# Performance work log

Hardware: AMD Instinct MI355X
Metric: run time of the kernel (lower is better)

## Reference

```python
import jax, jax.numpy as jnp
import numpy as np

D_MODEL = 1024
D_HEAD = 64
B, S = 4, 2048


def setup_inputs() -> dict:
    key = jax.random.key(0)
    k1, k2, k3, k4 = jax.random.split(key, 4)
    residual_stream = jax.random.normal(k1, (B, S, D_MODEL), dtype=jnp.float32)
    # torch.nn.Linear weights are [out_features, in_features]
    Wq = jax.random.normal(k2, (D_HEAD, D_MODEL), dtype=jnp.float32) * 0.02
    Wk = jax.random.normal(k3, (D_HEAD, D_MODEL), dtype=jnp.float32) * 0.02
    Wv = jax.random.normal(k4, (D_HEAD, D_MODEL), dtype=jnp.float32) * 0.02
    return {"residual_stream": residual_stream, "Wq": Wq, "Wk": Wk, "Wv": Wv}


def reference(residual_stream, Wq, Wk, Wv):
    # Linear projections (no bias): y = x @ W.T
    q = jnp.einsum('bsd,hd->bsh', residual_stream, Wq)  # [B,S,d_head]
    k = jnp.einsum('bsd,hd->bsh', residual_stream, Wk)
    v = jnp.einsum('bsd,hd->bsh', residual_stream, Wv)
    # NOTE: module scales by 1/sqrt(d_model), not 1/sqrt(d_head)
    scale = 1.0 / jnp.sqrt(jnp.float32(D_MODEL))
    scores = jnp.einsum('bqh,bkh->bqk', q, k) * scale  # [B,S,S]
    # causal mask: lower-triangular allowed
    s = residual_stream.shape[1]
    causal = jnp.tril(jnp.ones((s, s), dtype=bool))
    scores = jnp.where(causal[None, :, :], scores, -jnp.inf)
    attn = jax.nn.softmax(scores, axis=-1)
    # dropout_chance=0.0 (eval/deterministic) -> identity
    return jnp.einsum('bqk,bkh->bqh', attn, v)  # [B,S,d_head]
```

## Files before the change

kernel.cpp:

```cpp
#include <hip/hip_runtime.h>
#include <hip/hip_bf16.h>

#define NB 4
#define SEQ 2048
#define DM 1024
#define DH 64

typedef __attribute__((ext_vector_type(8))) short bf16x8;
typedef __attribute__((ext_vector_type(4))) float f32x4;
typedef __attribute__((ext_vector_type(4))) short short4v;

__device__ inline short f2bf(float f) {
  union { float f; unsigned u; } x; x.f = f;
  unsigned r = x.u + 0x7FFFu + ((x.u >> 16) & 1u);
  return (short)(r >> 16);
}

__device__ inline float bf2f(short s) {
  union { unsigned u; float f; } x;
  x.u = ((unsigned)(unsigned short)s) << 16;
  return x.f;
}

__global__ __launch_bounds__(256) void wconv_kernel(
    const float* __restrict__ Wq, const float* __restrict__ Wk,
    const float* __restrict__ Wv, short* __restrict__ wbf)
{
  const int tid = blockIdx.x * 256 + threadIdx.x;
  const int base = tid * 8;
  const int row = base >> 10;
  const int col = base & 1023;
  const float* src = (row < 64) ? Wq : (row < 128) ? Wk : Wv;
  src += (size_t)(row & 63) * DM + col;
  f32x4 f0 = ((const f32x4*)src)[0];
  f32x4 f1 = ((const f32x4*)src)[1];
  bf16x8 h = { f2bf(f0[0]), f2bf(f0[1]), f2bf(f0[2]), f2bf(f0[3]),
               f2bf(f1[0]), f2bf(f1[1]), f2bf(f1[2]), f2bf(f1[3]) };
  *(bf16x8*)(wbf + (size_t)row * DM + col) = h;
}

__global__ __launch_bounds__(512) void proj_v3_kernel(
    const float* __restrict__ X, const short* __restrict__ wbf,
    short* __restrict__ pacc)
{
  __shared__ short w_lds[192][264];
  __shared__ short x_lds[2][32][264];

  const int t = threadIdx.x;
  const int l = t & 63;
  const int w = t >> 6;
  const int ks = blockIdx.y;
  const int kbase = ks * 256;
  const int mbase = blockIdx.x * 128;

#pragma unroll
  for (int i = 0; i < 12; i++) {
    const int idx = t + i * 512;
    const int row = idx >> 5;
    const int cb = idx & 31;
    *(bf16x8*)&w_lds[row][cb * 8] =
        *(const bf16x8*)(wbf + (size_t)row * DM + kbase + cb * 8);
  }

  const int xr0 = t >> 6;
  const int xc0 = (t & 63) * 4;

  f32x4 xp0, xp1, xp2, xp3;
  {
    const float* base = X + (size_t)(mbase + xr0) * DM + kbase + xc0;
    xp0 = *(const f32x4*)(base + 0 * 8 * DM);
    xp1 = *(const f32x4*)(base + 1 * 8 * DM);
    xp2 = *(const f32x4*)(base + 2 * 8 * DM);
    xp3 = *(const f32x4*)(base + 3 * 8 * DM);
  }
  {
    short4v h0 = { f2bf(xp0[0]), f2bf(xp0[1]), f2bf(xp0[2]), f2bf(xp0[3]) };
    short4v h1 = { f2bf(xp1[0]), f2bf(xp1[1]), f2bf(xp1[2]), f2bf(xp1[3]) };
    short4v h2 = { f2bf(xp2[0]), f2bf(xp2[1]), f2bf(xp2[2]), f2bf(xp2[3]) };
    short4v h3 = { f2bf(xp3[0]), f2bf(xp3[1]), f2bf(xp3[2]), f2bf(xp3[3]) };
    *(short4v*)&x_lds[0][xr0 + 0][xc0]  = h0;
    *(short4v*)&x_lds[0][xr0 + 8][xc0]  = h1;
    *(short4v*)&x_lds[0][xr0 + 16][xc0] = h2;
    *(short4v*)&x_lds[0][xr0 + 24][xc0] = h3;
  }
  __syncthreads();

  const int arow = (w & 1) * 16 + (l & 15);
  const int kk = (l >> 4) << 3;
  const int cg = (w >> 1) * 3;
  short* pp = pacc + (size_t)ks * (NB * SEQ) * 192;

#pragma unroll
  for (int mt = 0; mt < 4; mt++) {
    const int buf = mt & 1;

    if (mt < 3) {
      const float* base = X + (size_t)(mbase + (mt + 1) * 32 + xr0) * DM + kbase + xc0;
      xp0 = *(const f32x4*)(base + 0 * 8 * DM);
      xp1 = *(const f32x4*)(base + 1 * 8 * DM);
      xp2 = *(const f32x4*)(base + 2 * 8 * DM);
      xp3 = *(const f32x4*)(base + 3 * 8 * DM);
    }

    f32x4 acc0 = (f32x4){0.f, 0.f, 0.f, 0.f};
    f32x4 acc1 = (f32x4){0.f, 0.f, 0.f, 0.f};
    f32x4 acc2 = (f32x4){0.f, 0.f, 0.f, 0.f};
#pragma unroll
    for (int k8 = 0; k8 < 8; k8++) {
      const int kc = k8 * 32 + kk;
      bf16x8 a  = *(const bf16x8*)&x_lds[buf][arow][kc];
      bf16x8 b0 = *(const bf16x8*)&w_lds[(cg + 0) * 16 + (l & 15)][kc];
      acc0 = __builtin_amdgcn_mfma_f32_16x16x32_bf16(a, b0, acc0, 0, 0, 0);
      bf16x8 b1 = *(const bf16x8*)&w_lds[(cg + 1) * 16 + (l & 15)][kc];
      acc1 = __builtin_amdgcn_mfma_f32_16x16x32_bf16(a, b1, acc1, 0, 0, 0);
      bf16x8 b2 = *(const bf16x8*)&w_lds[(cg + 2) * 16 + (l & 15)][kc];
      acc2 = __builtin_amdgcn_mfma_f32_16x16x32_bf16(a, b2, acc2, 0, 0, 0);
    }

    {
      const int rowb = mbase + mt * 32 + (w & 1) * 16 + ((l >> 4) << 2);
      const int c0 = (cg + 0) * 16 + (l & 15);
      const int c1 = (cg + 1) * 16 + (l & 15);
      const int c2 = (cg + 2) * 16 + (l & 15);
#pragma unroll
      for (int j = 0; j < 4; j++) {
        pp[(size_t)(rowb + j) * 192 + c0] = f2bf(acc0[j]);
        pp[(size_t)(rowb + j) * 192 + c1] = f2bf(acc1[j]);
        pp[(size_t)(rowb + j) * 192 + c2] = f2bf(acc2[j]);
      }
    }

    if (mt < 3) {
      short4v h0 = { f2bf(xp0[0]), f2bf(xp0[1]), f2bf(xp0[2]), f2bf(xp0[3]) };
      short4v h1 = { f2bf(xp1[0]), f2bf(xp1[1]), f2bf(xp1[2]), f2bf(xp1[3]) };
      short4v h2 = { f2bf(xp2[0]), f2bf(xp2[1]), f2bf(xp2[2]), f2bf(xp2[3]) };
      short4v h3 = { f2bf(xp3[0]), f2bf(xp3[1]), f2bf(xp3[2]), f2bf(xp3[3]) };
      *(short4v*)&x_lds[buf ^ 1][xr0 + 0][xc0]  = h0;
      *(short4v*)&x_lds[buf ^ 1][xr0 + 8][xc0]  = h1;
      *(short4v*)&x_lds[buf ^ 1][xr0 + 16][xc0] = h2;
      *(short4v*)&x_lds[buf ^ 1][xr0 + 24][xc0] = h3;
    }
    __syncthreads();
  }
}

__global__ __launch_bounds__(256) void reduce4_kernel(
    const short* __restrict__ pacc, short* __restrict__ qout,
    short* __restrict__ kout, short* __restrict__ vtout)
{
  const int gid = blockIdx.x * 256 + threadIdx.x;
  const int r = gid / 48;
  const int cg = gid - r * 48;
  const int c0 = cg * 4;

  float v0 = 0.f, v1 = 0.f, v2 = 0.f, v3 = 0.f;
#pragma unroll
  for (int s = 0; s < 4; s++) {
    const short4v a = *(const short4v*)(pacc + ((size_t)s * (NB * SEQ) + r) * 192 + c0);
    v0 += bf2f(a[0]); v1 += bf2f(a[1]); v2 += bf2f(a[2]); v3 += bf2f(a[3]);
  }

  if (c0 < 64) {
    short4v h = { f2bf(v0 * 0.03125f), f2bf(v1 * 0.03125f),
                  f2bf(v2 * 0.03125f), f2bf(v3 * 0.03125f) };
    *(short4v*)(qout + (size_t)r * DH + c0) = h;
  } else if (c0 < 128) {
    short4v h = { f2bf(v0), f2bf(v1), f2bf(v2), f2bf(v3) };
    *(short4v*)(kout + (size_t)r * DH + (c0 - 64)) = h;
  } else {
    const int bb = r >> 11, s = r & (SEQ - 1);
    short* vt = vtout + (size_t)bb * DH * SEQ + (size_t)(c0 - 128) * SEQ + s;
    vt[0 * SEQ] = f2bf(v0);
    vt[1 * SEQ] = f2bf(v1);
    vt[2 * SEQ] = f2bf(v2);
    vt[3 * SEQ] = f2bf(v3);
  }
}

__global__ __launch_bounds__(512) void proj_fb_kernel(
    const float* __restrict__ X, const short* __restrict__ wbf,
    short* __restrict__ qout, short* __restrict__ kout,
    short* __restrict__ vtout)
{
  __shared__ short x_lds[2][32][80];
  __shared__ short w_lds[2][192][80];

  const int t = threadIdx.x;
  const int l = t & 63;
  const int w = t >> 6;
  const int m0 = blockIdx.x * 32;

  f32x4 acc[3];
#pragma unroll
  for (int i = 0; i < 3; i++) acc[i] = (f32x4){0.f, 0.f, 0.f, 0.f};

  const int xr = t >> 4;
  const int xc = (t & 15) * 4;
  const int wr = t >> 3;
  const int wc = (t & 7) * 8;

  const float* xsrc  = X   + (size_t)(m0 + xr) * DM + xc;
  const short* wsrc0 = wbf + (size_t)(wr)       * DM + wc;
  const short* wsrc1 = wbf + (size_t)(64 + wr)  * DM + wc;
  const short* wsrc2 = wbf + (size_t)(128 + wr) * DM + wc;

  {
    f32x4 f = *(const f32x4*)xsrc;
    short4v h = { f2bf(f[0]), f2bf(f[1]), f2bf(f[2]), f2bf(f[3]) };
    *(short4v*)&x_lds[0][xr][xc] = h;
    *(bf16x8*)&w_lds[0][wr][wc]       = *(const bf16x8*)wsrc0;
    *(bf16x8*)&w_lds[0][64 + wr][wc]  = *(const bf16x8*)wsrc1;
    *(bf16x8*)&w_lds[0][128 + wr][wc] = *(const bf16x8*)wsrc2;
  }
  f32x4 xA = *(const f32x4*)(xsrc + 64);
  bf16x8 wA0 = *(const bf16x8*)(wsrc0 + 64);
  bf16x8 wA1 = *(const bf16x8*)(wsrc1 + 64);
  bf16x8 wA2 = *(const bf16x8*)(wsrc2 + 64);
  f32x4 xB;
  bf16x8 wB0, wB1, wB2;
  __syncthreads();

#pragma unroll
  for (int it = 0; it < 16; it++) {
    const int buf = it & 1;
    const int k2 = (it + 2) * 64;

    if ((it & 1) == 0) {
      if (it + 2 < 16) {
        xB  = *(const f32x4*)(xsrc + k2);
        wB0 = *(const bf16x8*)(wsrc0 + k2);
        wB1 = *(const bf16x8*)(wsrc1 + k2);
        wB2 = *(const bf16x8*)(wsrc2 + k2);
      }
    } else {
      if (it + 2 < 16) {
        xA  = *(const f32x4*)(xsrc + k2);
        wA0 = *(const bf16x8*)(wsrc0 + k2);
        wA1 = *(const bf16x8*)(wsrc1 + k2);
        wA2 = *(const bf16x8*)(wsrc2 + k2);
      }
    }

    const short* xp = &x_lds[buf][(w & 1) * 16 + (l & 15)][(l >> 4) << 3];
    bf16x8 a0 = *(const bf16x8*)xp;
    bf16x8 a1 = *(const bf16x8*)(xp + 32);
#pragma unroll
    for (int nf = 0; nf < 3; nf++) {
      const int cf = (w >> 1) * 3 + nf;
      const short* wp = &w_lds[buf][cf * 16 + (l & 15)][(l >> 4) << 3];
      bf16x8 b0 = *(const bf16x8*)wp;
      bf16x8 b1 = *(const bf16x8*)(wp + 32);
      acc[nf] = __builtin_amdgcn_mfma_f32_16x16x32_bf16(a0, b0, acc[nf], 0, 0, 0);
      acc[nf] = __builtin_amdgcn_mfma_f32_16x16x32_bf16(a1, b1, acc[nf], 0, 0, 0);
    }

    if (it < 15) {
      if ((it & 1) == 0) {
        short4v h = { f2bf(xA[0]), f2bf(xA[1]), f2bf(xA[2]), f2bf(xA[3]) };
        *(short4v*)&x_lds[buf ^ 1][xr][xc] = h;
        *(bf16x8*)&w_lds[buf ^ 1][wr][wc]       = wA0;
        *(bf16x8*)&w_lds[buf ^ 1][64 + wr][wc]  = wA1;
        *(bf16x8*)&w_lds[buf ^ 1][128 + wr][wc] = wA2;
      } else {
        short4v h = { f2bf(xB[0]), f2bf(xB[1]), f2bf(xB[2]), f2bf(xB[3]) };
        *(short4v*)&x_lds[buf ^ 1][xr][xc] = h;
        *(bf16x8*)&w_lds[buf ^ 1][wr][wc]       = wB0;
        *(bf16x8*)&w_lds[buf ^ 1][64 + wr][wc]  = wB1;
        *(bf16x8*)&w_lds[buf ^ 1][128 + wr][wc] = wB2;
      }
    }
    __syncthreads();
  }

  const int rowb = m0 + (w & 1) * 16 + ((l >> 4) << 2);
#pragma unroll
  for (int nf = 0; nf < 3; nf++) {
    const int c = ((w >> 1) * 3 + nf) * 16 + (l & 15);
#pragma unroll
    for (int j = 0; j < 4; j++) {
      const int row = rowb + j;
      const float v = acc[nf][j];
      if (c < 64) {
        qout[row * DH + c] = f2bf(v * 0.03125f);
      } else if (c < 128) {
        kout[row * DH + (c - 64)] = f2bf(v);
      } else {
        const int b = row >> 11, s = row & (SEQ - 1);
        vtout[b * (DH * SEQ) + (c - 128) * SEQ + s] = f2bf(v);
      }
    }
  }
}

__global__ __launch_bounds__(256) void flash_kernel(
    const short* __restrict__ qin, const short* __restrict__ kin,
    const short* __restrict__ vtin, float* __restrict__ po,
    float* __restrict__ pm, float* __restrict__ pl,
    const int nck, const int cht)
{
  __shared__ short k_lds[2][64][72];
  __shared__ short vt_lds[2][64][72];
  __shared__ short p_lds[4][16][72];

  const int qt = blockIdx.x;
  const int ck = blockIdx.y;
  const int t0 = ck * cht;
  if (t0 > qt) return;
  const int b = blockIdx.z;

  const int t = threadIdx.x;
  const int l = t & 63;
  const int w = t >> 6;
  const int q0 = qt * 64;
  const int tend = min(t0 + cht, qt + 1);

  const short* qb = qin  + (size_t)b * SEQ * DH;
  const short* kb = kin  + (size_t)b * SEQ * DH;
  const short* vb = vtin + (size_t)b * DH * SEQ;

  const short* qr = qb + (size_t)(q0 + w * 16 + (l & 15)) * DH + ((l >> 4) << 3);
  const bf16x8 qf0 = *(const bf16x8*)qr;
  const bf16x8 qf1 = *(const bf16x8*)(qr + 32);

  f32x4 o[4];
#pragma unroll
  for (int i = 0; i < 4; i++) o[i] = (f32x4){0.f, 0.f, 0.f, 0.f};
  float m_run[4] = {-1e30f, -1e30f, -1e30f, -1e30f};
  float l_run[4] = {0.f, 0.f, 0.f, 0.f};

  const int sr = t >> 3;
  const int sc = (t & 7) * 8;

  {
    const int j0 = t0 * 64;
#pragma unroll
    for (int i = 0; i < 2; i++) {
      const int r = sr + i * 32;
      *(bf16x8*)&k_lds[0][r][sc]  = *(const bf16x8*)(kb + (size_t)(j0 + r) * DH + sc);
      *(bf16x8*)&vt_lds[0][r][sc] = *(const bf16x8*)(vb + (size_t)r * SEQ + j0 + sc);
    }
  }
  __syncthreads();

  for (int tt = t0; tt < tend; tt++) {
    const int bi = (tt - t0) & 1;
    const int j0 = tt * 64;
    const bool pf = (tt + 1 < tend);

    bf16x8 kpf0, kpf1, vpf0, vpf1;
    if (pf) {
      const int j1 = j0 + 64;
      kpf0 = *(const bf16x8*)(kb + (size_t)(j1 + sr) * DH + sc);
      kpf1 = *(const bf16x8*)(kb + (size_t)(j1 + sr + 32) * DH + sc);
      vpf0 = *(const bf16x8*)(vb + (size_t)sr * SEQ + j1 + sc);
      vpf1 = *(const bf16x8*)(vb + (size_t)(sr + 32) * SEQ + j1 + sc);
    }

    f32x4 s[4];
#pragma unroll
    for (int nf = 0; nf < 4; nf++) {
      const short* kr = &k_lds[bi][nf * 16 + (l & 15)][(l >> 4) << 3];
      bf16x8 b0 = *(const bf16x8*)kr;
      bf16x8 b1 = *(const bf16x8*)(kr + 32);
      f32x4 a = (f32x4){0.f, 0.f, 0.f, 0.f};
      a = __builtin_amdgcn_mfma_f32_16x16x32_bf16(qf0, b0, a, 0, 0, 0);
      a = __builtin_amdgcn_mfma_f32_16x16x32_bf16(qf1, b1, a, 0, 0, 0);
      s[nf] = a;
    }

    {
      const int growb = q0 + w * 16 + ((l >> 4) << 2);
#pragma unroll
      for (int nf = 0; nf < 4; nf++) {
        const int gcol = j0 + nf * 16 + (l & 15);
#pragma unroll
        for (int j = 0; j < 4; j++)
          if (gcol > growb + j) s[nf][j] = -1e30f;
      }
    }

    float alpha[4];
#pragma unroll
    for (int j = 0; j < 4; j++) {
      float tm = fmaxf(fmaxf(s[0][j], s[1][j]), fmaxf(s[2][j], s[3][j]));
      tm = fmaxf(tm, __shfl_xor(tm, 1));
      tm = fmaxf(tm, __shfl_xor(tm, 2));
      tm = fmaxf(tm, __shfl_xor(tm, 4));
      tm = fmaxf(tm, __shfl_xor(tm, 8));
      const float mn = fmaxf(m_run[j], tm);
      alpha[j] = exp2f((m_run[j] - mn) * 1.44269504f);
      m_run[j] = mn;
      float rs = 0.f;
#pragma unroll
      for (int nf = 0; nf < 4; nf++) {
        const float p = exp2f((s[nf][j] - mn) * 1.44269504f);
        s[nf][j] = p;
        rs += p;
      }
      rs += __shfl_xor(rs, 1);
      rs += __shfl_xor(rs, 2);
      rs += __shfl_xor(rs, 4);
      rs += __shfl_xor(rs, 8);
      l_run[j] = l_run[j] * alpha[j] + rs;
    }
#pragma unroll
    for (int df = 0; df < 4; df++)
#pragma unroll
      for (int j = 0; j < 4; j++) o[df][j] *= alpha[j];

#pragma unroll
    for (int nf = 0; nf < 4; nf++)
#pragma unroll
      for (int j = 0; j < 4; j++)
        p_lds[w][((l >> 4) << 2) + j][nf * 16 + (l & 15)] = f2bf(s[nf][j]);

    asm volatile("s_waitcnt lgkmcnt(0)" ::: "memory");
    __builtin_amdgcn_sched_barrier(0);

#pragma unroll
    for (int ks = 0; ks < 2; ks++) {
      const short* pr = &p_lds[w][l & 15][ks * 32 + ((l >> 4) << 3)];
      const bf16x8 pa = *(const bf16x8*)pr;
#pragma unroll
      for (int df = 0; df < 4; df++) {
        const short* vr = &vt_lds[bi][df * 16 + (l & 15)][ks * 32 + ((l >> 4) << 3)];
        const bf16x8 vf = *(const bf16x8*)vr;
        o[df] = __builtin_amdgcn_mfma_f32_16x16x32_bf16(pa, vf, o[df], 0, 0, 0);
      }
    }

    if (pf) {
      *(bf16x8*)&k_lds[bi ^ 1][sr][sc]       = kpf0;
      *(bf16x8*)&k_lds[bi ^ 1][sr + 32][sc]  = kpf1;
      *(bf16x8*)&vt_lds[bi ^ 1][sr][sc]      = vpf0;
      *(bf16x8*)&vt_lds[bi ^ 1][sr + 32][sc] = vpf1;
    }
    __syncthreads();
  }

  const int rowb = q0 + w * 16 + ((l >> 4) << 2);
#pragma unroll
  for (int j = 0; j < 4; j++) {
    const size_t rowg = (size_t)b * SEQ + rowb + j;
#pragma unroll
    for (int df = 0; df < 4; df++)
      po[(rowg * nck + ck) * DH + df * 16 + (l & 15)] = o[df][j];
    if ((l & 15) == 0) {
      pm[rowg * nck + ck] = m_run[j];
      pl[rowg * nck + ck] = l_run[j];
    }
  }
}

__global__ __launch_bounds__(256) void merge_kernel(
    const float* __restrict__ po, const float* __restrict__ pm,
    const float* __restrict__ pl, float* __restrict__ out,
    const int nck, const int ckshift)
{
  const int gid = blockIdx.x * 256 + threadIdx.x;
  const int r = gid >> 6;
  const int d = gid & 63;
  const int s = r & (SEQ - 1);
  const int C = (s >> ckshift) + 1;

  float m = -1e30f;
  for (int c = 0; c < C; c++) m = fmaxf(m, pm[r * nck + c]);
  float den = 0.f, num = 0.f;
  for (int c = 0; c < C; c++) {
    const float wgt = exp2f((pm[r * nck + c] - m) * 1.44269504f);
    den += pl[r * nck + c] * wgt;
    num += po[(size_t)(r * nck + c) * DH + d] * wgt;
  }
  out[gid] = num / den;
}

extern "C" void kernel_launch(void* const* d_in, const int* in_sizes, int n_in,
                              void* d_out, int out_size, void* d_ws, size_t ws_size,
                              hipStream_t stream) {
  const float* X  = (const float*)d_in[0];
  const float* Wq = (const float*)d_in[1];
  const float* Wk = (const float*)d_in[2];
  const float* Wv = (const float*)d_in[3];

  const size_t nrow = (size_t)NB * SEQ;
  short* qws  = (short*)d_ws;
  short* kws  = qws + nrow * DH;
  short* vtws = kws + nrow * DH;
  const size_t qkv_bytes = 3 * nrow * DH * sizeof(short);

  const size_t big_need = qkv_bytes + 4 * nrow * 192 * sizeof(short)
                        + 192 * DM * sizeof(short);

  if (ws_size >= big_need) {
    short* pacc = vtws + nrow * DH;
    short* wbf  = pacc + 4 * nrow * 192;
    float* po   = (float*)pacc;
    float* pm   = po + nrow * 4 * DH;
    float* pl   = pm + nrow * 4;

    wconv_kernel<<<dim3(96), 256, 0, stream>>>(Wq, Wk, Wv, wbf);
    proj_v3_kernel<<<dim3(64, 4), 512, 0, stream>>>(X, wbf, pacc);
    reduce4_kernel<<<dim3((int)(nrow * 48 / 256)), 256, 0, stream>>>(pacc, qws, kws, vtws);
    flash_kernel<<<dim3(SEQ / 64, 4, NB), 256, 0, stream>>>(qws, kws, vtws, po, pm, pl, 4, 8);
    merge_kernel<<<dim3(NB * SEQ * DH / 256), 256, 0, stream>>>(po, pm, pl, (float*)d_out, 4, 9);
  } else {
    float* po  = (float*)(vtws + nrow * DH);
    short* wbf = (short*)po;

    int nck, cht, ckshift;
    const size_t need4 = qkv_bytes + nrow * 4 * (DH + 2) * sizeof(float);
    if (ws_size >= need4) { nck = 4; cht = 8;  ckshift = 9;  }
    else                  { nck = 1; cht = 32; ckshift = 11; }
    float* pm = po + nrow * nck * DH;
    float* pl = pm + nrow * nck;

    wconv_kernel<<<dim3(96), 256, 0, stream>>>(Wq, Wk, Wv, wbf);
    proj_fb_kernel<<<dim3(NB * SEQ / 32), 512, 0, stream>>>(X, wbf, qws, kws, vtws);
    flash_kernel<<<dim3(SEQ / 64, nck, NB), 256, 0, stream>>>(qws, kws, vtws, po, pm, pl, nck, cht);
    merge_kernel<<<dim3(NB * SEQ * DH / 256), 256, 0, stream>>>(po, pm, pl, (float*)d_out, nck, ckshift);
  }
}
```

Before: 55.72 us.

## Restructure projection kernel: per-wave 16x192 tiles, direct X loads, swizzled W LDS

The split-K projection kernel drops the double-buffered X staging through LDS and its per-subtile syncs. Each wave now loads its own 16 rows of X straight from global memory, converts them to bf16 in registers, and computes all 12 output column fragments with 12 accumulators. Weights sit in an unpadded LDS tile with an XOR swizzle to avoid bank conflicts. This removes the LDS traffic and barriers for X at the cost of more accumulator registers and unstaged global X loads. The fallback kernel's LDS padding also changes, but that path is not taken with the default workspace.

```diff
diff --git a/kernel.cpp b/kernel.cpp
--- a/kernel.cpp
+++ b/kernel.cpp
@@ -39,108 +39,61 @@
   *(bf16x8*)(wbf + (size_t)row * DM + col) = h;
 }
 
-__global__ __launch_bounds__(512) void proj_v3_kernel(
+__global__ __launch_bounds__(512) void proj_v5_kernel(
     const float* __restrict__ X, const short* __restrict__ wbf,
     short* __restrict__ pacc)
 {
-  __shared__ short w_lds[192][264];
-  __shared__ short x_lds[2][32][264];
+  __shared__ short w_lds[192 * 256];
 
   const int t = threadIdx.x;
   const int l = t & 63;
   const int w = t >> 6;
   const int ks = blockIdx.y;
   const int kbase = ks * 256;
-  const int mbase = blockIdx.x * 128;
+  const int m0 = blockIdx.x * 128;
 
 #pragma unroll
   for (int i = 0; i < 12; i++) {
     const int idx = t + i * 512;
     const int row = idx >> 5;
-    const int cb = idx & 31;
-    *(bf16x8*)&w_lds[row][cb * 8] =
-        *(const bf16x8*)(wbf + (size_t)row * DM + kbase + cb * 8);
-  }
-
-  const int xr0 = t >> 6;
-  const int xc0 = (t & 63) * 4;
-
-  f32x4 xp0, xp1, xp2, xp3;
-  {
-    const float* base = X + (size_t)(mbase + xr0) * DM + kbase + xc0;
-    xp0 = *(const f32x4*)(base + 0 * 8 * DM);
-    xp1 = *(const f32x4*)(base + 1 * 8 * DM);
-    xp2 = *(const f32x4*)(base + 2 * 8 * DM);
-    xp3 = *(const f32x4*)(base + 3 * 8 * DM);
-  }
-  {
-    short4v h0 = { f2bf(xp0[0]), f2bf(xp0[1]), f2bf(xp0[2]), f2bf(xp0[3]) };
-    short4v h1 = { f2bf(xp1[0]), f2bf(xp1[1]), f2bf(xp1[2]), f2bf(xp1[3]) };
-    short4v h2 = { f2bf(xp2[0]), f2bf(xp2[1]), f2bf(xp2[2]), f2bf(xp2[3]) };
-    short4v h3 = { f2bf(xp3[0]), f2bf(xp3[1]), f2bf(xp3[2]), f2bf(xp3[3]) };
-    *(short4v*)&x_lds[0][xr0 + 0][xc0]  = h0;
-    *(short4v*)&x_lds[0][xr0 + 8][xc0]  = h1;
-    *(short4v*)&x_lds[0][xr0 + 16][xc0] = h2;
-    *(short4v*)&x_lds[0][xr0 + 24][xc0] = h3;
+    const int c = idx & 31;
+    bf16x8 v = *(const bf16x8*)(wbf + (size_t)row * DM + kbase + c * 8);
+    const int cs = (c & ~7) | ((c ^ row) & 7);
+    *(bf16x8*)&w_lds[row * 256 + cs * 8] = v;
   }
   __syncthreads();
 
-  const int arow = (w & 1) * 16 + (l & 15);
-  const int kk = (l >> 4) << 3;
-  const int cg = (w >> 1) * 3;
+  f32x4 acc[12];
+#pragma unroll
+  for (int i = 0; i < 12; i++) acc[i] = (f32x4){0.f, 0.f, 0.f, 0.f};
+
+  const float* xrow = X + (size_t)(m0 + w * 16 + (l & 15)) * DM
+                        + kbase + ((l >> 4) << 3);
+
+#pragma unroll
+  for (int k8 = 0; k8 < 8; k8++) {
+    f32x4 xa0 = *(const f32x4*)(xrow + k8 * 32);
+    f32x4 xa1 = *(const f32x4*)(xrow + k8 * 32 + 4);
+    bf16x8 a = { f2bf(xa0[0]), f2bf(xa0[1]), f2bf(xa0[2]), f2bf(xa0[3]),
+                 f2bf(xa1[0]), f2bf(xa1[1]), f2bf(xa1[2]), f2bf(xa1[3]) };
+    const int c = k8 * 4 + (l >> 4);
+#pragma unroll
+    for (int nf = 0; nf < 12; nf++) {
+      const int row = nf * 16 + (l & 15);
+      const int cs = (c & ~7) | ((c ^ row) & 7);
+      bf16x8 b = *(const bf16x8*)&w_lds[row * 256 + cs * 8];
+      acc[nf] = __builtin_amdgcn_mfma_f32_16x16x32_bf16(a, b, acc[nf], 0, 0, 0);
+    }
+  }
+
   short* pp = pacc + (size_t)ks * (NB * SEQ) * 192;
-
-#pragma unroll
-  for (int mt = 0; mt < 4; mt++) {
-    const int buf = mt & 1;
-
-    if (mt < 3) {
-      const float* base = X + (size_t)(mbase + (mt + 1) * 32 + xr0) * DM + kbase + xc0;
-      xp0 = *(const f32x4*)(base + 0 * 8 * DM);
-      xp1 = *(const f32x4*)(base + 1 * 8 * DM);
-      xp2 = *(const f32x4*)(base + 2 * 8 * DM);
-      xp3 = *(const f32x4*)(base + 3 * 8 * DM);
-    }
-
-    f32x4 acc0 = (f32x4){0.f, 0.f, 0.f, 0.f};
-    f32x4 acc1 = (f32x4){0.f, 0.f, 0.f, 0.f};
-    f32x4 acc2 = (f32x4){0.f, 0.f, 0.f, 0.f};
-#pragma unroll
-    for (int k8 = 0; k8 < 8; k8++) {
-      const int kc = k8 * 32 + kk;
-      bf16x8 a  = *(const bf16x8*)&x_lds[buf][arow][kc];
-      bf16x8 b0 = *(const bf16x8*)&w_lds[(cg + 0) * 16 + (l & 15)][kc];
-      acc0 = __builtin_amdgcn_mfma_f32_16x16x32_bf16(a, b0, acc0, 0, 0, 0);
-      bf16x8 b1 = *(const bf16x8*)&w_lds[(cg + 1) * 16 + (l & 15)][kc];
-      acc1 = __builtin_amdgcn_mfma_f32_16x16x32_bf16(a, b1, acc1, 0, 0, 0);
-      bf16x8 b2 = *(const bf16x8*)&w_lds[(cg + 2) * 16 + (l & 15)][kc];
-      acc2 = __builtin_amdgcn_mfma_f32_16x16x32_bf16(a, b2, acc2, 0, 0, 0);
-    }
-
-    {
-      const int rowb = mbase + mt * 32 + (w & 1) * 16 + ((l >> 4) << 2);
-      const int c0 = (cg + 0) * 16 + (l & 15);
-      const int c1 = (cg + 1) * 16 + (l & 15);
-      const int c2 = (cg + 2) * 16 + (l & 15);
-#pragma unroll
-      for (int j = 0; j < 4; j++) {
-        pp[(size_t)(rowb + j) * 192 + c0] = f2bf(acc0[j]);
-        pp[(size_t)(rowb + j) * 192 + c1] = f2bf(acc1[j]);
-        pp[(size_t)(rowb + j) * 192 + c2] = f2bf(acc2[j]);
-      }
-    }
-
-    if (mt < 3) {
-      short4v h0 = { f2bf(xp0[0]), f2bf(xp0[1]), f2bf(xp0[2]), f2bf(xp0[3]) };
-      short4v h1 = { f2bf(xp1[0]), f2bf(xp1[1]), f2bf(xp1[2]), f2bf(xp1[3]) };
-      short4v h2 = { f2bf(xp2[0]), f2bf(xp2[1]), f2bf(xp2[2]), f2bf(xp2[3]) };
-      short4v h3 = { f2bf(xp3[0]), f2bf(xp3[1]), f2bf(xp3[2]), f2bf(xp3[3]) };
-      *(short4v*)&x_lds[buf ^ 1][xr0 + 0][xc0]  = h0;
-      *(short4v*)&x_lds[buf ^ 1][xr0 + 8][xc0]  = h1;
-      *(short4v*)&x_lds[buf ^ 1][xr0 + 16][xc0] = h2;
-      *(short4v*)&x_lds[buf ^ 1][xr0 + 24][xc0] = h3;
-    }
-    __syncthreads();
+  const int rowb = m0 + w * 16 + ((l >> 4) << 2);
+#pragma unroll
+  for (int nf = 0; nf < 12; nf++) {
+    const int c = nf * 16 + (l & 15);
+#pragma unroll
+    for (int j = 0; j < 4; j++)
+      pp[(size_t)(rowb + j) * 192 + c] = f2bf(acc[nf][j]);
   }
 }
 
@@ -182,8 +135,8 @@
     short* __restrict__ qout, short* __restrict__ kout,
     short* __restrict__ vtout)
 {
-  __shared__ short x_lds[2][32][80];
-  __shared__ short w_lds[2][192][80];
+  __shared__ short x_lds[2][32][72];
+  __shared__ short w_lds[2][192][72];
 
   const int t = threadIdx.x;
   const int l = t & 63;
@@ -499,7 +452,7 @@
     float* pl   = pm + nrow * 4;
 
     wconv_kernel<<<dim3(96), 256, 0, stream>>>(Wq, Wk, Wv, wbf);
-    proj_v3_kernel<<<dim3(64, 4), 512, 0, stream>>>(X, wbf, pacc);
+    proj_v5_kernel<<<dim3(64, 4), 512, 0, stream>>>(X, wbf, pacc);
     reduce4_kernel<<<dim3((int)(nrow * 48 / 256)), 256, 0, stream>>>(pacc, qws, kws, vtws);
     flash_kernel<<<dim3(SEQ / 64, 4, NB), 256, 0, stream>>>(qws, kws, vtws, po, pm, pl, 4, 8);
     merge_kernel<<<dim3(NB * SEQ * DH / 256), 256, 0, stream>>>(po, pm, pl, (float*)d_out, 4, 9);
```

New measurement: 54.48 us. -2.2%, faster.
